# Performance work log

Hardware: AMD Instinct MI355X
Metric: run time of the kernel (lower is better)

The kernel has to match this reference:

```python
import jax, jax.numpy as jnp
import numpy as np


def setup_inputs() -> dict:
    key = jax.random.key(0)
    k1, k2 = jax.random.split(key)
    inputs = jax.random.normal(k1, (16, 64, 64, 64), dtype=jnp.float32)  # NCHW, C=embedding_dim
    codebook = jax.random.normal(k2, (1024, 64), dtype=jnp.float32)      # [K, D]
    return {"inputs": inputs, "codebook": codebook}


def reference(inputs, codebook):
    # inputs: [B, C, H, W] -> [B, H, W, C] -> [N, D]
    D = codebook.shape[1]
    x = jnp.transpose(inputs, (0, 2, 3, 1)).reshape(-1, D)  # [N, D]
    distances = (
        jnp.sum(x * x, axis=1, keepdims=True)
        + jnp.sum(codebook * codebook, axis=1)
        - 2.0 * jnp.matmul(x, codebook.T)
    )
    encoding_indices = jnp.argmin(distances, axis=1)[:, None]  # [N, 1]
    return encoding_indices
```

## Files before the change

kernel.cpp:

```cpp
#include <hip/hip_runtime.h>


typedef float f4 __attribute__((ext_vector_type(4)));
typedef float f32x16 __attribute__((ext_vector_type(16)));
typedef short s8v __attribute__((ext_vector_type(8)));
typedef unsigned int u32;

#define D_DIM 64
#define HW    4096
#define ROWSB 128
#define INF_  __builtin_inff()
#define M32(a,b,c) __builtin_amdgcn_mfma_f32_32x32x16_bf16(a,b,c,0,0,0)
#define Z16 (f32x16){0.f,0.f,0.f,0.f,0.f,0.f,0.f,0.f,0.f,0.f,0.f,0.f,0.f,0.f,0.f,0.f}

__device__ __forceinline__ unsigned short bf_rne(float f) {
    u32 u = __builtin_bit_cast(u32, f);
    u32 r = u + 0x7fffu + ((u >> 16) & 1u);
    return (unsigned short)(r >> 16);
}
__device__ __forceinline__ float bf_to_f(unsigned short h) {
    u32 u = ((u32)h) << 16;
    return __builtin_bit_cast(float, u);
}
__device__ __forceinline__ void split3(float f, unsigned short& h,
                                       unsigned short& m, unsigned short& l) {
    h = bf_rne(f);
    float f1 = f - bf_to_f(h);
    m = bf_rne(f1);
    float f2 = f1 - bf_to_f(m);
    l = bf_rne(f2);
}
__device__ __forceinline__ s8v pack8(unsigned short a0, unsigned short a1,
                                     unsigned short a2, unsigned short a3,
                                     unsigned short a4, unsigned short a5,
                                     unsigned short a6, unsigned short a7) {
    uint4 u;
    u.x = a0 | ((u32)a1 << 16);
    u.y = a2 | ((u32)a3 << 16);
    u.z = a4 | ((u32)a5 << 16);
    u.w = a6 | ((u32)a7 << 16);
    return __builtin_bit_cast(s8v, u);
}

__global__ __launch_bounds__(64) void prep_kernel(const float* __restrict__ cb,
                                                  char* __restrict__ wsb) {
    const int blk = blockIdx.x;
    const int lane = threadIdx.x;
    if (blk < 384) {
        const int T = blk / 12;
        const int rem = blk - T * 12;
        const int s = rem / 3;
        const int L = rem - s * 3;
        const int code = T * 32 + (lane & 31);
        const int ch0 = s * 16 + (lane >> 5) * 8;
        const float* src = cb + code * 64 + ch0;
        unsigned short o[8];
#pragma unroll
        for (int j = 0; j < 8; ++j) {
            unsigned short h, m2, l;
            split3(src[j], h, m2, l);
            o[j] = (L == 0) ? h : (L == 1) ? m2 : l;
        }
        uint4 w;
        w.x = o[0] | ((u32)o[1] << 16);
        w.y = o[2] | ((u32)o[3] << 16);
        w.z = o[4] | ((u32)o[5] << 16);
        w.w = o[6] | ((u32)o[7] << 16);
        *(uint4*)(wsb + (size_t)blk * 1024 + lane * 16) = w;
    } else {
        const int k = (blk - 384) * 64 + lane;
        const f4* row = (const f4*)(cb + (size_t)k * 64);
        float sacc = 0.f;
#pragma unroll
        for (int i = 0; i < 16; ++i) {
            f4 v = row[i];
            sacc = fmaf(v.x, v.x, sacc);
            sacc = fmaf(v.y, v.y, sacc);
            sacc = fmaf(v.z, v.z, sacc);
            sacc = fmaf(v.w, v.w, sacc);
        }
        ((float*)(wsb + 384 * 1024))[k] = sacc;
    }
}

__device__ __forceinline__ void gl_lds16(const char* g, char* l) {
    __builtin_amdgcn_global_load_lds(
        (const __attribute__((address_space(1))) void*)g,
        (__attribute__((address_space(3))) void*)l, 16, 0, 0);
}

#define BUILD_A(s) { \
    const float* xr = (const float*)&xs4[w32 + l31][0]; \
    f4 va = *(const f4*)(xr + (s) * 16 + lh8); \
    f4 vb = *(const f4*)(xr + (s) * 16 + lh8 + 4); \
    unsigned short h0,h1,h2,h3,h4,h5,h6,h7; \
    unsigned short q0,q1,q2,q3,q4,q5,q6,q7; \
    unsigned short l0,l1,l2,l3,l4,l5,l6,l7; \
    split3(-2.f * va.x, h0, q0, l0); split3(-2.f * va.y, h1, q1, l1); \
    split3(-2.f * va.z, h2, q2, l2); split3(-2.f * va.w, h3, q3, l3); \
    split3(-2.f * vb.x, h4, q4, l4); split3(-2.f * vb.y, h5, q5, l5); \
    split3(-2.f * vb.z, h6, q6, l6); split3(-2.f * vb.w, h7, q7, l7); \
    Ah##s = pack8(h0,h1,h2,h3,h4,h5,h6,h7); \
    Am##s = pack8(q0,q1,q2,q3,q4,q5,q6,q7); \
    Al##s = pack8(l0,l1,l2,l3,l4,l5,l6,l7); \
}

#define QUAD(la, lb) \
    c0 = M32(A##la##0, B0##lb, c0); c1 = M32(A##la##1, B1##lb, c1); \
    c2 = M32(A##la##2, B2##lb, c2); c3 = M32(A##la##3, B3##lb, c3);

#define UPD(i) { \
    float v = sv[i] + en0; \
    bool pr = (v < best##i); \
    best##i = pr ? v : best##i; \
    idx##i  = pr ? kn0 : idx##i; \
}

#define BF1(i, msk) { \
    float ov = __shfl_xor(best##i, msk); \
    int   oi = __shfl_xor(idx##i,  msk); \
    bool pr = (ov < best##i) || (ov == best##i && oi < idx##i); \
    best##i = pr ? ov : best##i; \
    idx##i  = pr ? oi : idx##i; \
}
#define BFALL(msk) \
    BF1(0,msk)  BF1(1,msk)  BF1(2,msk)  BF1(3,msk) \
    BF1(4,msk)  BF1(5,msk)  BF1(6,msk)  BF1(7,msk) \
    BF1(8,msk)  BF1(9,msk)  BF1(10,msk) BF1(11,msk) \
    BF1(12,msk) BF1(13,msk) BF1(14,msk) BF1(15,msk)

__global__ __launch_bounds__(256, 2) void vq_kernel(const float* __restrict__ x,
                                                    const char* __restrict__ wsb,
                                                    int* __restrict__ out) {
    __shared__ __align__(16) char smem[36864];
    __shared__ float sEn[1024];
    f4 (*xs4)[17] = (f4 (*)[17])smem;
    char* const sB = smem;

    const int tid = threadIdx.x;
    const int lane = tid & 63;
    const int w = __builtin_amdgcn_readfirstlane(tid >> 6);
    const int l31 = lane & 31;
    const int lh = lane >> 5;
    const int lh8 = lh * 8;
    const int w32 = w * 32;
    const int wu = w * 3072;
    const int lane16 = lane * 16;
    const int stageoff = wu + lane16;
    const int n0 = blockIdx.x * ROWSB;
    const int b = n0 >> 12;
    const int hw0 = n0 & (HW - 1);

    const float* enp = (const float*)(wsb + 384 * 1024);
#pragma unroll
    for (int q = 0; q < 4; ++q) sEn[q * 256 + tid] = enp[q * 256 + tid];

    {
        const float* g = x + ((size_t)b * D_DIM + w * 16) * HW + hw0 + lane;
        float v[16], v2[16];
#pragma unroll
        for (int i = 0; i < 16; ++i) { v[i] = g[(size_t)i * HW]; v2[i] = g[(size_t)i * HW + 64]; }
#pragma unroll
        for (int j = 0; j < 4; ++j) {
            xs4[lane][w * 4 + j]      = (f4){v[4*j],  v[4*j+1],  v[4*j+2],  v[4*j+3]};
            xs4[lane + 64][w * 4 + j] = (f4){v2[4*j], v2[4*j+1], v2[4*j+2], v2[4*j+3]};
        }
    }
    __syncthreads();

    s8v Ah0, Am0, Al0, Ah1, Am1, Al1, Ah2, Am2, Al2, Ah3, Am3, Al3;
    BUILD_A(0) BUILD_A(1) BUILD_A(2) BUILD_A(3)
    __syncthreads();

    char* b0 = sB;
    char* b1 = sB + 12288;
    char* b2 = sB + 24576;

    gl_lds16(wsb + stageoff,                b0 + wu);
    gl_lds16(wsb + stageoff + 1024,         b0 + wu + 1024);
    gl_lds16(wsb + stageoff + 2048,         b0 + wu + 2048);
    gl_lds16(wsb + 12288 + stageoff,        b1 + wu);
    gl_lds16(wsb + 12288 + stageoff + 1024, b1 + wu + 1024);
    gl_lds16(wsb + 12288 + stageoff + 2048, b1 + wu + 2048);

    float best0=INF_, best1=INF_, best2=INF_, best3=INF_;
    float best4=INF_, best5=INF_, best6=INF_, best7=INF_;
    float best8=INF_, best9=INF_, best10=INF_, best11=INF_;
    float best12=INF_, best13=INF_, best14=INF_, best15=INF_;
    int idx0=0, idx1=0, idx2=0, idx3=0, idx4=0, idx5=0, idx6=0, idx7=0;
    int idx8=0, idx9=0, idx10=0, idx11=0, idx12=0, idx13=0, idx14=0, idx15=0;

    asm volatile("s_waitcnt vmcnt(3)" ::: "memory");
    __builtin_amdgcn_s_barrier();

    const char* gp = wsb + 2 * 12288;
    const char* const gend = wsb + 32 * 12288;
    int p32 = 0;

#pragma unroll 1
    for (int pp = 0; pp < 32; ++pp) {
        gl_lds16(gp + stageoff,        b2 + wu);
        gl_lds16(gp + stageoff + 1024, b2 + wu + 1024);
        gl_lds16(gp + stageoff + 2048, b2 + wu + 2048);

        const char* bb = b0 + lane16;
        s8v B0h = *(const s8v*)(bb +     0), B0m = *(const s8v*)(bb +  1024);
        s8v B0l = *(const s8v*)(bb +  2048);
        s8v B1h = *(const s8v*)(bb +  3072), B1m = *(const s8v*)(bb +  4096);
        s8v B1l = *(const s8v*)(bb +  5120);
        s8v B2h = *(const s8v*)(bb +  6144), B2m = *(const s8v*)(bb +  7168);
        s8v B2l = *(const s8v*)(bb +  8192);
        s8v B3h = *(const s8v*)(bb +  9216), B3m = *(const s8v*)(bb + 10240);
        s8v B3l = *(const s8v*)(bb + 11264);
        const float en0 = sEn[p32 + l31];

        f32x16 c0 = Z16, c1 = Z16, c2 = Z16, c3 = Z16;
        __builtin_amdgcn_s_setprio(1);
        QUAD(h,h) QUAD(h,m) QUAD(m,h) QUAD(h,l) QUAD(m,m) QUAD(l,h)
        __builtin_amdgcn_s_setprio(0);

        f32x16 sv = (c0 + c1) + (c2 + c3);
        const int kn0 = p32 + l31;
        UPD(0)  UPD(1)  UPD(2)  UPD(3)  UPD(4)  UPD(5)  UPD(6)  UPD(7)
        UPD(8)  UPD(9)  UPD(10) UPD(11) UPD(12) UPD(13) UPD(14) UPD(15)

        asm volatile("s_waitcnt vmcnt(3) lgkmcnt(0)" ::: "memory");
        __builtin_amdgcn_s_barrier();

        { char* t = b0; b0 = b1; b1 = b2; b2 = t; }
        gp += 12288;
        if (gp == gend) gp = wsb;
        p32 += 32;
    }
    asm volatile("s_waitcnt vmcnt(0)" ::: "memory");

    BFALL(1) BFALL(2) BFALL(4) BFALL(8) BFALL(16)

    if (l31 == 0) {
        int* op = out + n0 + w32 + lh * 4;
        int4 q0; q0.x = idx0;  q0.y = idx1;  q0.z = idx2;  q0.w = idx3;
        int4 q1; q1.x = idx4;  q1.y = idx5;  q1.z = idx6;  q1.w = idx7;
        int4 q2; q2.x = idx8;  q2.y = idx9;  q2.z = idx10; q2.w = idx11;
        int4 q3; q3.x = idx12; q3.y = idx13; q3.z = idx14; q3.w = idx15;
        *(int4*)(op)      = q0;
        *(int4*)(op + 8)  = q1;
        *(int4*)(op + 16) = q2;
        *(int4*)(op + 24) = q3;
    }
}

extern "C" void kernel_launch(void* const* d_in, const int* in_sizes, int n_in,
                              void* d_out, int out_size, void* d_ws, size_t ws_size,
                              hipStream_t stream) {
    const float* x  = (const float*)d_in[0];
    const float* cb = (const float*)d_in[1];
    char* wsb = (char*)d_ws;
    int*  out = (int*)d_out;

    prep_kernel<<<dim3(400), dim3(64), 0, stream>>>(cb, wsb);
    vq_kernel<<<dim3(65536 / ROWSB), dim3(256), 0, stream>>>(x, wsb, out);
}
```

Before: 116.5 us.

## Software-pipeline argmin update and seed MFMA accumulator with codebook norms

Moves the argmin compare/select for each codebook chunk one iteration later, so it runs while the next chunk's MFMAs are in flight instead of waiting on their results. It also starts the accumulator at the codebook-norm value, which removes the separate add, and reorders the six split-precision MFMAs per k-slice into two accumulator chains instead of four. Fewer chains means longer dependent MFMA sequences, which may expose MFMA latency, and the deferred update adds a carried vector register plus an extra update after the loop. The changed summation order could shift near-tie results slightly.

Measured after the change: 112.8 us. -3.2%, faster.

```diff
diff --git a/kernel.cpp b/kernel.cpp
--- a/kernel.cpp
+++ b/kernel.cpp
@@ -105,16 +105,19 @@
     Al##s = pack8(l0,l1,l2,l3,l4,l5,l6,l7); \
 }
 
-#define QUAD(la, lb) \
-    c0 = M32(A##la##0, B0##lb, c0); c1 = M32(A##la##1, B1##lb, c1); \
-    c2 = M32(A##la##2, B2##lb, c2); c3 = M32(A##la##3, B3##lb, c3);
+#define K6(s) \
+    c0 = M32(Ah##s, B##s##h, c0); c1 = M32(Ah##s, B##s##m, c1); \
+    c0 = M32(Am##s, B##s##h, c0); c1 = M32(Ah##s, B##s##l, c1); \
+    c0 = M32(Am##s, B##s##m, c0); c1 = M32(Al##s, B##s##h, c1);
 
 #define UPD(i) { \
-    float v = sv[i] + en0; \
-    bool pr = (v < best##i); \
-    best##i = pr ? v : best##i; \
-    idx##i  = pr ? kn0 : idx##i; \
-}
+    bool pr = (svp[i] < best##i); \
+    best##i = pr ? svp[i] : best##i; \
+    idx##i  = pr ? kprev : idx##i; \
+}
+#define UPD_ALL \
+    UPD(0)  UPD(1)  UPD(2)  UPD(3)  UPD(4)  UPD(5)  UPD(6)  UPD(7) \
+    UPD(8)  UPD(9)  UPD(10) UPD(11) UPD(12) UPD(13) UPD(14) UPD(15)
 
 #define BF1(i, msk) { \
     float ov = __shfl_xor(best##i, msk); \
@@ -190,6 +193,11 @@
     int idx0=0, idx1=0, idx2=0, idx3=0, idx4=0, idx5=0, idx6=0, idx7=0;
     int idx8=0, idx9=0, idx10=0, idx11=0, idx12=0, idx13=0, idx14=0, idx15=0;
 
+    f32x16 svp;
+#pragma unroll
+    for (int i = 0; i < 16; ++i) svp[i] = INF_;
+    int kprev = 0;
+
     asm volatile("s_waitcnt vmcnt(3)" ::: "memory");
     __builtin_amdgcn_s_barrier();
 
@@ -214,15 +222,18 @@
         s8v B3l = *(const s8v*)(bb + 11264);
         const float en0 = sEn[p32 + l31];
 
-        f32x16 c0 = Z16, c1 = Z16, c2 = Z16, c3 = Z16;
+        f32x16 c0, c1 = Z16;
+#pragma unroll
+        for (int i = 0; i < 16; ++i) c0[i] = en0;
+
         __builtin_amdgcn_s_setprio(1);
-        QUAD(h,h) QUAD(h,m) QUAD(m,h) QUAD(h,l) QUAD(m,m) QUAD(l,h)
+        K6(0) K6(1) K6(2) K6(3)
         __builtin_amdgcn_s_setprio(0);
 
-        f32x16 sv = (c0 + c1) + (c2 + c3);
-        const int kn0 = p32 + l31;
-        UPD(0)  UPD(1)  UPD(2)  UPD(3)  UPD(4)  UPD(5)  UPD(6)  UPD(7)
-        UPD(8)  UPD(9)  UPD(10) UPD(11) UPD(12) UPD(13) UPD(14) UPD(15)
+        UPD_ALL
+
+        svp = c0 + c1;
+        kprev = p32 + l31;
 
         asm volatile("s_waitcnt vmcnt(3) lgkmcnt(0)" ::: "memory");
         __builtin_amdgcn_s_barrier();
@@ -233,6 +244,8 @@
         p32 += 32;
     }
     asm volatile("s_waitcnt vmcnt(0)" ::: "memory");
+
+    UPD_ALL
 
     BFALL(1) BFALL(2) BFALL(4) BFALL(8) BFALL(16)
 
```

## Software-pipeline MFMA and argmin update with double-buffered accumulators

Applied to the files above, without the earlier changes.

Restructures the main loop into two alternating phases, each with its own pair of accumulators. The argmin update for the previous tile now runs while the current tile's MFMAs execute, and a final update handles the last tile after the loop. The codebook norm is preloaded into the accumulator, so no separate add is needed. The accumulator count drops from four to two chains, which shortens the reduction but lengthens each dependent MFMA chain. Staggering the LDS B loads is meant to overlap them with compute, at the cost of more live registers under the 256,2 launch bound.

Result: faster. 110.8 us (-4.9%).

```diff
diff --git a/kernel.cpp b/kernel.cpp
--- a/kernel.cpp
+++ b/kernel.cpp
@@ -105,15 +105,53 @@
     Al##s = pack8(l0,l1,l2,l3,l4,l5,l6,l7); \
 }
 
-#define QUAD(la, lb) \
-    c0 = M32(A##la##0, B0##lb, c0); c1 = M32(A##la##1, B1##lb, c1); \
-    c2 = M32(A##la##2, B2##lb, c2); c3 = M32(A##la##3, B3##lb, c3);
-
-#define UPD(i) { \
-    float v = sv[i] + en0; \
+#define U1(QS, i) { \
+    float v = QS##0[i] + QS##1[i]; \
     bool pr = (v < best##i); \
     best##i = pr ? v : best##i; \
-    idx##i  = pr ? kn0 : idx##i; \
+    idx##i  = pr ? kn : idx##i; \
+}
+#define UPDS(QS) \
+    U1(QS,0)  U1(QS,1)  U1(QS,2)  U1(QS,3)  U1(QS,4)  U1(QS,5)  U1(QS,6)  U1(QS,7) \
+    U1(QS,8)  U1(QS,9)  U1(QS,10) U1(QS,11) U1(QS,12) U1(QS,13) U1(QS,14) U1(QS,15)
+
+#define PH(PS, QS) { \
+    gl_lds16(gp + stageoff,        b2 + wu); \
+    gl_lds16(gp + stageoff + 1024, b2 + wu + 1024); \
+    gl_lds16(gp + stageoff + 2048, b2 + wu + 2048); \
+    const char* bb = b0 + lane16; \
+    const float en0 = sEn[p32 + l31]; \
+    _Pragma("unroll") \
+    for (int _i = 0; _i < 16; ++_i) PS##0[_i] = en0; \
+    PS##1 = Z16; \
+    s8v B0h = *(const s8v*)(bb +     0), B0m = *(const s8v*)(bb +  1024); \
+    s8v B0l = *(const s8v*)(bb +  2048); \
+    s8v B1h = *(const s8v*)(bb +  3072), B1m = *(const s8v*)(bb +  4096); \
+    s8v B1l = *(const s8v*)(bb +  5120); \
+    PS##0 = M32(Ah0,B0h,PS##0); PS##1 = M32(Ah0,B0m,PS##1); \
+    PS##0 = M32(Am0,B0h,PS##0); PS##1 = M32(Ah0,B0l,PS##1); \
+    PS##0 = M32(Am0,B0m,PS##0); PS##1 = M32(Al0,B0h,PS##1); \
+    PS##0 = M32(Ah1,B1h,PS##0); PS##1 = M32(Ah1,B1m,PS##1); \
+    PS##0 = M32(Am1,B1h,PS##0); PS##1 = M32(Ah1,B1l,PS##1); \
+    PS##0 = M32(Am1,B1m,PS##0); PS##1 = M32(Al1,B1h,PS##1); \
+    s8v B2h = *(const s8v*)(bb +  6144), B2m = *(const s8v*)(bb +  7168); \
+    s8v B2l = *(const s8v*)(bb +  8192); \
+    s8v B3h = *(const s8v*)(bb +  9216), B3m = *(const s8v*)(bb + 10240); \
+    s8v B3l = *(const s8v*)(bb + 11264); \
+    PS##0 = M32(Ah2,B2h,PS##0); PS##1 = M32(Ah2,B2m,PS##1); \
+    PS##0 = M32(Am2,B2h,PS##0); PS##1 = M32(Ah2,B2l,PS##1); \
+    PS##0 = M32(Am2,B2m,PS##0); PS##1 = M32(Al2,B2h,PS##1); \
+    PS##0 = M32(Ah3,B3h,PS##0); PS##1 = M32(Ah3,B3m,PS##1); \
+    PS##0 = M32(Am3,B3h,PS##0); PS##1 = M32(Ah3,B3l,PS##1); \
+    PS##0 = M32(Am3,B3m,PS##0); PS##1 = M32(Al3,B3h,PS##1); \
+    { const int kn = p32 - 32 + l31; UPDS(QS) } \
+    asm volatile("s_waitcnt vmcnt(3) lgkmcnt(0)" ::: "memory"); \
+    __builtin_amdgcn_s_barrier(); \
+    asm volatile("" ::: "memory"); \
+    { char* t = b0; b0 = b1; b1 = b2; b2 = t; } \
+    gp += 12288; \
+    if (gp == gend) gp = wsb; \
+    p32 += 32; \
 }
 
 #define BF1(i, msk) { \
@@ -190,49 +228,27 @@
     int idx0=0, idx1=0, idx2=0, idx3=0, idx4=0, idx5=0, idx6=0, idx7=0;
     int idx8=0, idx9=0, idx10=0, idx11=0, idx12=0, idx13=0, idx14=0, idx15=0;
 
+    f32x16 cp0, cp1;
+    f32x16 cq0, cq1 = Z16;
+#pragma unroll
+    for (int i = 0; i < 16; ++i) cq0[i] = INF_;
+
     asm volatile("s_waitcnt vmcnt(3)" ::: "memory");
     __builtin_amdgcn_s_barrier();
+    asm volatile("" ::: "memory");
 
     const char* gp = wsb + 2 * 12288;
     const char* const gend = wsb + 32 * 12288;
     int p32 = 0;
 
 #pragma unroll 1
-    for (int pp = 0; pp < 32; ++pp) {
-        gl_lds16(gp + stageoff,        b2 + wu);
-        gl_lds16(gp + stageoff + 1024, b2 + wu + 1024);
-        gl_lds16(gp + stageoff + 2048, b2 + wu + 2048);
-
-        const char* bb = b0 + lane16;
-        s8v B0h = *(const s8v*)(bb +     0), B0m = *(const s8v*)(bb +  1024);
-        s8v B0l = *(const s8v*)(bb +  2048);
-        s8v B1h = *(const s8v*)(bb +  3072), B1m = *(const s8v*)(bb +  4096);
-        s8v B1l = *(const s8v*)(bb +  5120);
-        s8v B2h = *(const s8v*)(bb +  6144), B2m = *(const s8v*)(bb +  7168);
-        s8v B2l = *(const s8v*)(bb +  8192);
-        s8v B3h = *(const s8v*)(bb +  9216), B3m = *(const s8v*)(bb + 10240);
-        s8v B3l = *(const s8v*)(bb + 11264);
-        const float en0 = sEn[p32 + l31];
-
-        f32x16 c0 = Z16, c1 = Z16, c2 = Z16, c3 = Z16;
-        __builtin_amdgcn_s_setprio(1);
-        QUAD(h,h) QUAD(h,m) QUAD(m,h) QUAD(h,l) QUAD(m,m) QUAD(l,h)
-        __builtin_amdgcn_s_setprio(0);
-
-        f32x16 sv = (c0 + c1) + (c2 + c3);
-        const int kn0 = p32 + l31;
-        UPD(0)  UPD(1)  UPD(2)  UPD(3)  UPD(4)  UPD(5)  UPD(6)  UPD(7)
-        UPD(8)  UPD(9)  UPD(10) UPD(11) UPD(12) UPD(13) UPD(14) UPD(15)
-
-        asm volatile("s_waitcnt vmcnt(3) lgkmcnt(0)" ::: "memory");
-        __builtin_amdgcn_s_barrier();
-
-        { char* t = b0; b0 = b1; b1 = b2; b2 = t; }
-        gp += 12288;
-        if (gp == gend) gp = wsb;
-        p32 += 32;
+    for (int pp = 0; pp < 16; ++pp) {
+        PH(cp, cq)
+        PH(cq, cp)
     }
     asm volatile("s_waitcnt vmcnt(0)" ::: "memory");
+
+    { const int kn = p32 - 32 + l31; UPDS(cq) }
 
     BFALL(1) BFALL(2) BFALL(4) BFALL(8) BFALL(16)
 
```
